# Kernel optimization log

Measured on AMD Instinct MI355X. Metric: run time of the kernel, lower is better.

Reference implementation:

```python
import jax, jax.numpy as jnp
import numpy as np

B, S, E = 2, 2048, 1024
G, Q, D = 4, 4, 64          # n_groups, queries-per-group, head dim
SCALE = 1.0 / np.sqrt(E).astype(np.float32)  # sequence_attention=False -> 1/sqrt(embed_dim)


def setup_inputs() -> dict:
    key = jax.random.key(0)
    ks = jax.random.split(key, 12)
    init = lambda k, shp, fan_in: jax.random.uniform(k, shp, jnp.float32, -1.0, 1.0) / np.sqrt(fan_in)
    return {
        "q": jax.random.normal(ks[0], (B, S, E), jnp.float32),
        "k": jax.random.normal(ks[1], (B, S, E), jnp.float32),
        "v": jax.random.normal(ks[2], (B, S, E), jnp.float32),
        "Wq_w": init(ks[3], (E, G * Q * D), E),
        "Wq_b": init(ks[4], (G * Q * D,), E),
        "Wk_w": init(ks[5], (E, G * D), E),
        "Wk_b": init(ks[6], (G * D,), E),
        "Wv_w": init(ks[7], (E, G * D), E),
        "Wv_b": init(ks[8], (G * D,), E),
        "fc_w": init(ks[9], (G * Q * D, G * Q * D), G * Q * D),
        "fc_b": init(ks[10], (G * Q * D,), G * Q * D),
    }


def reference(q, k, v, Wq_w, Wq_b, Wk_w, Wk_b, Wv_w, Wv_b, fc_w, fc_b):
    # projections
    qh = (q @ Wq_w + Wq_b).reshape(B, S, G, Q, D)   # b s g q d
    kh = (k @ Wk_w + Wk_b).reshape(B, S, G, D)      # b s g d (1 KV head per group)
    vh = (v @ Wv_w + Wv_b).reshape(B, S, G, D)
    # energy: broadcast single KV head across Q query heads per group
    energy = jnp.einsum('bsgqd,btgd->bgqst', qh, kh) * SCALE  # [b,g,q,s,s]
    attn = jax.nn.softmax(energy, axis=-1)
    out = jnp.einsum('bgqst,btgd->bsgqd', attn, vh)           # b s g q d
    out = out.reshape(B, S, G * Q * D)                        # b s (g q d)
    return out @ fc_w + fc_b
```

## Files before the change

kernel.cpp:

```cpp
#include <hip/hip_runtime.h>


typedef unsigned short u16;
typedef __attribute__((ext_vector_type(4))) unsigned short u16x4;
typedef __attribute__((ext_vector_type(8))) short bf16x8;
typedef __attribute__((ext_vector_type(8))) unsigned short u16x8;
typedef __attribute__((ext_vector_type(4))) float f32x4;
typedef __attribute__((ext_vector_type(8))) float f32x8;

#define MFMA16(a, b, c) __builtin_amdgcn_mfma_f32_16x16x32_bf16(a, b, c, 0, 0, 0)

#define SC2L 0.045084140608f

__device__ __forceinline__ u16 f2b(float f) {
  unsigned int i = __builtin_bit_cast(unsigned int, f);
  i += 0x7fffu + ((i >> 16) & 1u);
  return (u16)(i >> 16);
}
__device__ __forceinline__ unsigned cvtpk_bf16(float a, float b) {
  unsigned r;
  asm("v_cvt_pk_bf16_f32 %0, %1, %2" : "=v"(r) : "v"(a), "v"(b));
  return r;
}
__device__ __forceinline__ void gload_lds16(const u16* g, u16* l) {
  __builtin_amdgcn_global_load_lds(
      (const __attribute__((address_space(1))) unsigned int*)g,
      (__attribute__((address_space(3))) unsigned int*)l, 16, 0, 0);
}

__global__ __launch_bounds__(256) void transpose_all(const float* __restrict__ Wq_w,
                                                     const float* __restrict__ Wk_w,
                                                     const float* __restrict__ Wv_w,
                                                     const float* __restrict__ fc_w,
                                                     u16* __restrict__ WqT,
                                                     u16* __restrict__ WkT,
                                                     u16* __restrict__ WvT,
                                                     u16* __restrict__ fcT) {
  __shared__ u16 tile[32][33];
  int r = blockIdx.x;
  const float* W; u16* Wt; int N; float scale;
  if (r < 1024)      { W = Wq_w; Wt = WqT; N = 1024; scale = SC2L; }
  else if (r < 1280) { W = Wk_w; Wt = WkT; N = 256;  scale = 1.0f; r -= 1024; }
  else if (r < 1536) { W = Wv_w; Wt = WvT; N = 256;  scale = 1.0f; r -= 1280; }
  else               { W = fc_w; Wt = fcT; N = 1024; scale = 1.0f; r -= 1536; }
  const int K = 1024;
  const int bk = (r & 31) * 32;
  const int bn = (r >> 5) * 32;
  const int tx = threadIdx.x & 31, ty = threadIdx.x >> 5;
#pragma unroll
  for (int rr = ty; rr < 32; rr += 8)
    tile[rr][tx] = f2b(W[(size_t)(bk + rr) * N + bn + tx] * scale);
  __syncthreads();
#pragma unroll
  for (int rr = ty; rr < 32; rr += 8) Wt[(size_t)(bn + rr) * K + bk + tx] = tile[tx][rr];
}

template <typename AT, typename CT>
__device__ __forceinline__ void gemm_body(const AT* __restrict__ A,
                                          const u16* __restrict__ Bt,
                                          const float* __restrict__ bias,
                                          CT* __restrict__ C,
                                          int M, int N, int K, float bscale,
                                          bool transv, int bid) {
  __shared__ alignas(16) u16 As[2][64 * 32];
  __shared__ alignas(16) u16 Bs[2][128 * 32];
  const int tid = threadIdx.x;
  const int lane = tid & 63, wave = tid >> 6;
  const int l15 = lane & 15, lg = lane >> 4;
  const int nb = N >> 7;
  const int bm = (bid / nb) << 6;
  const int bn = (bid % nb) << 7;
  const int wr = (wave >> 2) << 5;
  const int wc = (wave & 3) << 5;
  const int crow = tid >> 2;
  const int ccol = (tid & 3) * 8;
  const AT*  arow = A  + (size_t)(bm + crow) * K + ccol;
  const u16* brow = Bt + (size_t)(bn + crow) * K + ccol;

  f32x4 acc[2][2] = {};
  const int nt = K >> 5;

  if (tid < 256) {
    if constexpr (__is_same(AT, float)) {
      const f32x8 af0 = *(const f32x8*)(arow);
      u16x8 av; unsigned* aw = (unsigned*)&av;
#pragma unroll
      for (int j = 0; j < 4; ++j) aw[j] = cvtpk_bf16(af0[2 * j], af0[2 * j + 1]);
      *(u16x8*)(As[0] + tid * 8) = av;
    } else {
      gload_lds16(arow, As[0] + tid * 8);
    }
  }
  gload_lds16(brow, Bs[0] + tid * 8);
  __syncthreads();

#pragma unroll 2
  for (int t = 0; t < nt; ++t) {
    const int c = t & 1;
    const int k1 = (t + 1) << 5;
    f32x8 afn;
    if (t + 1 < nt) {
      if (tid < 256) {
        if constexpr (__is_same(AT, float)) {
          afn = *(const f32x8*)(arow + k1);
        } else {
          gload_lds16(arow + k1, As[c ^ 1] + tid * 8);
        }
      }
      gload_lds16(brow + k1, Bs[c ^ 1] + tid * 8);
    }

    bf16x8 af[2], bf[2];
#pragma unroll
    for (int m = 0; m < 2; ++m)
      af[m] = *(const bf16x8*)(As[c] + (wr + m * 16 + l15) * 32 + lg * 8);
#pragma unroll
    for (int n = 0; n < 2; ++n)
      bf[n] = *(const bf16x8*)(Bs[c] + (wc + n * 16 + l15) * 32 + lg * 8);
#pragma unroll
    for (int m = 0; m < 2; ++m)
#pragma unroll
      for (int n = 0; n < 2; ++n) acc[m][n] = MFMA16(af[m], bf[n], acc[m][n]);

    if constexpr (__is_same(AT, float)) {
      if (t + 1 < nt && tid < 256) {
        u16x8 av; unsigned* aw = (unsigned*)&av;
#pragma unroll
        for (int j = 0; j < 4; ++j) aw[j] = cvtpk_bf16(afn[2 * j], afn[2 * j + 1]);
        *(u16x8*)(As[c ^ 1] + tid * 8) = av;
      }
    }
    __syncthreads();
  }

  float bvv[2];
#pragma unroll
  for (int n = 0; n < 2; ++n) bvv[n] = bias[bn + wc + n * 16 + l15] * bscale;

  if (transv) {
#pragma unroll
    for (int m = 0; m < 2; ++m) {
      const int row = bm + wr + m * 16 + lg * 4;
      const int bb = row >> 11, t = row & 2047;
#pragma unroll
      for (int n = 0; n < 2; ++n) {
        const int col = bn + wc + n * 16 + l15;
        u16x4 pk;
#pragma unroll
        for (int rr = 0; rr < 4; ++rr) pk[rr] = f2b(acc[m][n][rr] + bvv[n]);
        *(u16x4*)(C + (size_t)bb * ((size_t)N * 2048) + (size_t)col * 2048 + t) = pk;
      }
    }
  } else {
#pragma unroll
    for (int m = 0; m < 2; ++m) {
      const int row = bm + wr + m * 16 + lg * 4;
#pragma unroll
      for (int rr = 0; rr < 4; ++rr) {
        CT* cp = C + (size_t)(row + rr) * N + bn + wc + l15;
#pragma unroll
        for (int n = 0; n < 2; ++n) {
          const float val = acc[m][n][rr] + bvv[n];
          if constexpr (__is_same(CT, u16)) cp[n * 16] = f2b(val);
          else                              cp[n * 16] = val;
        }
      }
    }
  }
}

__global__ __launch_bounds__(512, 4) void gemm_qkv(const float* __restrict__ q,
                                                   const float* __restrict__ k,
                                                   const float* __restrict__ v,
                                                   const u16* __restrict__ WqT,
                                                   const u16* __restrict__ WkT,
                                                   const u16* __restrict__ WvT,
                                                   const float* __restrict__ Wq_b,
                                                   const float* __restrict__ Wk_b,
                                                   const float* __restrict__ Wv_b,
                                                   u16* __restrict__ qh,
                                                   u16* __restrict__ kh,
                                                   u16* __restrict__ vt) {
  if (blockIdx.x < 512)
    gemm_body<float, u16>(q, WqT, Wq_b, qh, 4096, 1024, 1024, SC2L, false, blockIdx.x);
  else if (blockIdx.x < 640)
    gemm_body<float, u16>(k, WkT, Wk_b, kh, 4096, 256, 1024, 1.0f, false, blockIdx.x - 512);
  else
    gemm_body<float, u16>(v, WvT, Wv_b, vt, 4096, 256, 1024, 1.0f, true, blockIdx.x - 640);
}

template <typename AT, typename CT, bool TRANSV>
__global__ __launch_bounds__(512, 4) void gemm_bt_bias(const AT* __restrict__ A,
                                                       const u16* __restrict__ Bt,
                                                       const float* __restrict__ bias,
                                                       CT* __restrict__ C,
                                                       int M, int N, int K, float bscale) {
  gemm_body<AT, CT>(A, Bt, bias, C, M, N, K, bscale, TRANSV, blockIdx.x);
}

__global__ __launch_bounds__(512, 2) void attn_fwd(const u16* __restrict__ qh,
                                                   const u16* __restrict__ kh,
                                                   const u16* __restrict__ vhT,
                                                   u16* __restrict__ ao) {
  constexpr int S = 2048;
  __shared__ alignas(16) u16 Klds[2][128][72];
  __shared__ alignas(16) u16 Vt[2][64][136];

  const int tid = threadIdx.x;
  const int lane = tid & 63, w = tid >> 6;
  const int h = w & 3, ssub = w >> 2;
  const int l15 = lane & 15, lg = lane >> 4;
  const int bid = blockIdx.x;
  const int s0 = (bid & 31) << 6;
  const int g = (bid >> 5) & 3;
  const int b = bid >> 7;
  const int sbase = s0 + ssub * 32;

  bf16x8 qf[2][2];
#pragma unroll
  for (int sh = 0; sh < 2; ++sh) {
    const u16* qrow = qh + (((size_t)(b * S + sbase + sh * 16 + l15)) << 10)
                      + g * 256 + h * 64 + lg * 8;
    qf[sh][0] = *(const bf16x8*)(qrow);
    qf[sh][1] = *(const bf16x8*)(qrow + 32);
  }

  const u16* kbase = kh + (((size_t)(b * S)) << 8) + g * 64;
  const u16* vtbase = vhT + ((size_t)(b * 256 + g * 64)) * 2048;

  float lsum[2] = {0.f, 0.f};
  f32x4 o[2][4] = {};

  const int srow = tid >> 3;
  const int sdp = (tid & 7) * 8;
  const int sig = (srow & 32) | (((srow >> 2) & 1) << 4) | (((srow >> 3) & 3) << 2) | (srow & 3);
  const int vrow = tid >> 4;
  const int vcol = (tid & 15) * 8;

  u16x8 kv[2], vv[2];
#define LOADTILE(T0)                                                                   \
  do {                                                                                 \
    kv[0] = *(const u16x8*)(kbase + (size_t)((T0) + srow) * 256 + sdp);                \
    kv[1] = *(const u16x8*)(kbase + (size_t)((T0) + 64 + srow) * 256 + sdp);           \
    vv[0] = *(const u16x8*)(vtbase + (size_t)vrow * 2048 + (T0) + vcol);               \
    vv[1] = *(const u16x8*)(vtbase + (size_t)(vrow + 32) * 2048 + (T0) + vcol);        \
  } while (0)

  LOADTILE(0);

#pragma unroll 2
  for (int i = 0; i < 16; ++i) {
    const int c = i & 1;
    *(u16x8*)(&Klds[c][sig][sdp])       = kv[0];
    *(u16x8*)(&Klds[c][sig + 64][sdp])  = kv[1];
    *(u16x8*)(&Vt[c][vrow][vcol])       = vv[0];
    *(u16x8*)(&Vt[c][vrow + 32][vcol])  = vv[1];
    __syncthreads();
    if (i + 1 < 16) LOADTILE((i + 1) << 7);

#pragma unroll
    for (int tt = 0; tt < 2; ++tt) {
#pragma unroll
      for (int kk = 0; kk < 2; ++kk) {
        float p[2][8];
#pragma unroll
        for (int nn = 0; nn < 2; ++nn) {
          const int n = kk * 2 + nn;
          const bf16x8 bk0 = *(const bf16x8*)(&Klds[c][tt * 64 + n * 16 + l15][lg * 8]);
          const bf16x8 bk1 = *(const bf16x8*)(&Klds[c][tt * 64 + n * 16 + l15][32 + lg * 8]);
          __builtin_amdgcn_s_setprio(1);
#pragma unroll
          for (int sh = 0; sh < 2; ++sh) {
            f32x4 z = {};
            z = MFMA16(bk0, qf[sh][0], z);
            z = MFMA16(bk1, qf[sh][1], z);
            __builtin_amdgcn_s_setprio(0);
#pragma unroll
            for (int r = 0; r < 4; ++r) {
              const float pv = exp2f(z[r]);
              lsum[sh] += pv;
              p[sh][nn * 4 + r] = pv;
            }
          }
        }
        bf16x8 pa[2];
#pragma unroll
        for (int sh = 0; sh < 2; ++sh) {
          unsigned* paw = (unsigned*)&pa[sh];
          paw[0] = cvtpk_bf16(p[sh][0], p[sh][1]);
          paw[1] = cvtpk_bf16(p[sh][2], p[sh][3]);
          paw[2] = cvtpk_bf16(p[sh][4], p[sh][5]);
          paw[3] = cvtpk_bf16(p[sh][6], p[sh][7]);
        }
        __builtin_amdgcn_s_setprio(1);
#pragma unroll
        for (int nd = 0; nd < 4; ++nd) {
          const bf16x8 bv = *(const bf16x8*)(&Vt[c][nd * 16 + l15][tt * 64 + kk * 32 + lg * 8]);
          o[0][nd] = MFMA16(pa[0], bv, o[0][nd]);
          o[1][nd] = MFMA16(pa[1], bv, o[1][nd]);
        }
        __builtin_amdgcn_s_setprio(0);
      }
    }
  }
#undef LOADTILE

#pragma unroll
  for (int sh = 0; sh < 2; ++sh) {
    float rs = lsum[sh];
    rs += __shfl_xor(rs, 16, 64);
    rs += __shfl_xor(rs, 32, 64);
    const float inv = 1.f / rs;
#pragma unroll
    for (int r = 0; r < 4; ++r) {
      const float invr = __shfl(inv, lg * 4 + r, 64);
      u16* orow = ao + (((size_t)(b * S + sbase + sh * 16 + lg * 4 + r)) << 10)
                  + g * 256 + h * 64 + l15;
#pragma unroll
      for (int nd = 0; nd < 4; ++nd) orow[nd * 16] = f2b(o[sh][nd][r] * invr);
    }
  }
}

extern "C" void kernel_launch(void* const* d_in, const int* in_sizes, int n_in,
                              void* d_out, int out_size, void* d_ws, size_t ws_size,
                              hipStream_t stream) {
  const float* q    = (const float*)d_in[0];
  const float* k    = (const float*)d_in[1];
  const float* v    = (const float*)d_in[2];
  const float* Wq_w = (const float*)d_in[3];
  const float* Wq_b = (const float*)d_in[4];
  const float* Wk_w = (const float*)d_in[5];
  const float* Wk_b = (const float*)d_in[6];
  const float* Wv_w = (const float*)d_in[7];
  const float* Wv_b = (const float*)d_in[8];
  const float* fc_w = (const float*)d_in[9];
  const float* fc_b = (const float*)d_in[10];
  float* out = (float*)d_out;

  u16* ws  = (u16*)d_ws;
  u16* WqT = ws;
  u16* WkT = WqT + 1024 * 1024;
  u16* WvT = WkT + 256 * 1024;
  u16* fcT = WvT + 256 * 1024;
  u16* qhp = fcT + 1024 * 1024;
  u16* khp = qhp + 4096 * 1024;
  u16* vtp = khp + 4096 * 256;
  u16* aop = vtp + 4096 * 256;

  transpose_all<<<2560, 256, 0, stream>>>(Wq_w, Wk_w, Wv_w, fc_w, WqT, WkT, WvT, fcT);

  gemm_qkv<<<768, 512, 0, stream>>>(q, k, v, WqT, WkT, WvT, Wq_b, Wk_b, Wv_b,
                                    qhp, khp, vtp);

  attn_fwd<<<256, 512, 0, stream>>>(qhp, khp, vtp, aop);

  gemm_bt_bias<u16, float, false><<<512, 512, 0, stream>>>(aop, fcT, fc_b, out, 4096, 1024, 1024, 1.0f);
}
```

Baseline: 113.5 us.

## Split attention over key dimension into two halves with combine kernel

Splits each attention block's key/value range into two halves, doubling the grid from 256 to 512 blocks so the GPU's compute units are better filled. Each half writes unnormalized bf16 partial outputs and row sums to workspace, and a new combine kernel adds the two partials and normalizes before the output GEMM. This works without max rescaling because the code uses a fixed-offset softmax. The cost is an extra kernel launch, extra workspace traffic, and an added bf16 rounding of the partial sums.

```diff
diff --git a/kernel.cpp b/kernel.cpp
--- a/kernel.cpp
+++ b/kernel.cpp
@@ -9,13 +9,16 @@
 typedef __attribute__((ext_vector_type(8))) float f32x8;
 
 #define MFMA16(a, b, c) __builtin_amdgcn_mfma_f32_16x16x32_bf16(a, b, c, 0, 0, 0)
-
 #define SC2L 0.045084140608f
 
 __device__ __forceinline__ u16 f2b(float f) {
   unsigned int i = __builtin_bit_cast(unsigned int, f);
   i += 0x7fffu + ((i >> 16) & 1u);
   return (u16)(i >> 16);
+}
+__device__ __forceinline__ float b2f(u16 u) {
+  unsigned int i = ((unsigned int)u) << 16;
+  return __builtin_bit_cast(float, i);
 }
 __device__ __forceinline__ unsigned cvtpk_bf16(float a, float b) {
   unsigned r;
@@ -198,10 +201,11 @@
   gemm_body<AT, CT>(A, Bt, bias, C, M, N, K, bscale, TRANSV, blockIdx.x);
 }
 
-__global__ __launch_bounds__(512, 2) void attn_fwd(const u16* __restrict__ qh,
+__global__ __launch_bounds__(512, 4) void attn_fwd(const u16* __restrict__ qh,
                                                    const u16* __restrict__ kh,
                                                    const u16* __restrict__ vhT,
-                                                   u16* __restrict__ ao) {
+                                                   u16* __restrict__ ows,
+                                                   float* __restrict__ lws) {
   constexpr int S = 2048;
   __shared__ alignas(16) u16 Klds[2][128][72];
   __shared__ alignas(16) u16 Vt[2][64][136];
@@ -213,7 +217,8 @@
   const int bid = blockIdx.x;
   const int s0 = (bid & 31) << 6;
   const int g = (bid >> 5) & 3;
-  const int b = bid >> 7;
+  const int th = (bid >> 7) & 1;
+  const int b = bid >> 8;
   const int sbase = s0 + ssub * 32;
 
   bf16x8 qf[2][2];
@@ -225,8 +230,8 @@
     qf[sh][1] = *(const bf16x8*)(qrow + 32);
   }
 
-  const u16* kbase = kh + (((size_t)(b * S)) << 8) + g * 64;
-  const u16* vtbase = vhT + ((size_t)(b * 256 + g * 64)) * 2048;
+  const u16* kbase = kh + (((size_t)(b * S)) << 8) + g * 64 + ((size_t)th << 10) * 256;
+  const u16* vtbase = vhT + ((size_t)(b * 256 + g * 64)) * 2048 + (th << 10);
 
   float lsum[2] = {0.f, 0.f};
   f32x4 o[2][4] = {};
@@ -249,14 +254,14 @@
   LOADTILE(0);
 
 #pragma unroll 2
-  for (int i = 0; i < 16; ++i) {
+  for (int i = 0; i < 8; ++i) {
     const int c = i & 1;
     *(u16x8*)(&Klds[c][sig][sdp])       = kv[0];
     *(u16x8*)(&Klds[c][sig + 64][sdp])  = kv[1];
     *(u16x8*)(&Vt[c][vrow][vcol])       = vv[0];
     *(u16x8*)(&Vt[c][vrow + 32][vcol])  = vv[1];
     __syncthreads();
-    if (i + 1 < 16) LOADTILE((i + 1) << 7);
+    if (i + 1 < 8) LOADTILE((i + 1) << 7);
 
 #pragma unroll
     for (int tt = 0; tt < 2; ++tt) {
@@ -305,21 +310,38 @@
   }
 #undef LOADTILE
 
+  u16* owsp = ows + ((size_t)th << 22);
+  float* lwsp = lws + (th << 16);
 #pragma unroll
   for (int sh = 0; sh < 2; ++sh) {
     float rs = lsum[sh];
     rs += __shfl_xor(rs, 16, 64);
     rs += __shfl_xor(rs, 32, 64);
-    const float inv = 1.f / rs;
+    if (lane < 16)
+      lwsp[((size_t)(b * S + sbase + sh * 16 + lane)) * 16 + g * 4 + h] = rs;
 #pragma unroll
     for (int r = 0; r < 4; ++r) {
-      const float invr = __shfl(inv, lg * 4 + r, 64);
-      u16* orow = ao + (((size_t)(b * S + sbase + sh * 16 + lg * 4 + r)) << 10)
+      u16* orow = owsp + (((size_t)(b * S + sbase + sh * 16 + lg * 4 + r)) << 10)
                   + g * 256 + h * 64 + l15;
 #pragma unroll
-      for (int nd = 0; nd < 4; ++nd) orow[nd * 16] = f2b(o[sh][nd][r] * invr);
-    }
-  }
+      for (int nd = 0; nd < 4; ++nd) orow[nd * 16] = f2b(o[sh][nd][r]);
+    }
+  }
+}
+
+__global__ __launch_bounds__(256) void attn_combine(u16* __restrict__ ows,
+                                                    const float* __restrict__ lws) {
+  const size_t i = ((size_t)blockIdx.x * 256 + threadIdx.x) * 8;
+  const int row = (int)(i >> 10);
+  const int gh = ((int)i & 1023) >> 6;
+  const float l = lws[(size_t)row * 16 + gh] + lws[(size_t)65536 + (size_t)row * 16 + gh];
+  const float inv = 1.f / l;
+  const u16x8 a = *(const u16x8*)(ows + i);
+  const u16x8 bb = *(const u16x8*)(ows + ((size_t)1 << 22) + i);
+  u16x8 r;
+#pragma unroll
+  for (int j = 0; j < 8; ++j) r[j] = f2b((b2f(a[j]) + b2f(bb[j])) * inv);
+  *(u16x8*)(ows + i) = r;
 }
 
 extern "C" void kernel_launch(void* const* d_in, const int* in_sizes, int n_in,
@@ -346,14 +368,16 @@
   u16* qhp = fcT + 1024 * 1024;
   u16* khp = qhp + 4096 * 1024;
   u16* vtp = khp + 4096 * 256;
-  u16* aop = vtp + 4096 * 256;
+  u16* owp = vtp + 4096 * 256;
+  float* lwp = (float*)(owp + 2 * 4096 * 1024);
 
   transpose_all<<<2560, 256, 0, stream>>>(Wq_w, Wk_w, Wv_w, fc_w, WqT, WkT, WvT, fcT);
 
   gemm_qkv<<<768, 512, 0, stream>>>(q, k, v, WqT, WkT, WvT, Wq_b, Wk_b, Wv_b,
                                     qhp, khp, vtp);
 
-  attn_fwd<<<256, 512, 0, stream>>>(qhp, khp, vtp, aop);
-
-  gemm_bt_bias<u16, float, false><<<512, 512, 0, stream>>>(aop, fcT, fc_b, out, 4096, 1024, 1024, 1.0f);
-}
+  attn_fwd<<<512, 512, 0, stream>>>(qhp, khp, vtp, owp, lwp);
+  attn_combine<<<2048, 256, 0, stream>>>(owp, lwp);
+
+  gemm_bt_bias<u16, float, false><<<512, 512, 0, stream>>>(owp, fcT, fc_b, out, 4096, 1024, 1024, 1.0f);
+}
```

Result: slower. 138.2 us (+21.7%).
